# Kernel optimization log

Hardware: AMD Instinct MI355X
Metric: run time of the kernel (lower is better)

The kernel has to match this reference:

```python
import jax, jax.numpy as jnp
import numpy as np
import math

B, S, E, H, D = 2, 2048, 1024, 16, 64

def setup_inputs() -> dict:
    key = jax.random.key(0)
    ks = jax.random.split(key, 9)
    sc = 0.02
    return {
        "x": jax.random.normal(ks[0], (B, S, E), jnp.float32),
        "Wq": jax.random.normal(ks[1], (H, E, D), jnp.float32) * sc,
        "Wk": jax.random.normal(ks[2], (H, E, D), jnp.float32) * sc,
        "Wv": jax.random.normal(ks[3], (H, E, D), jnp.float32) * sc,
        "bq": jax.random.normal(ks[4], (H, D), jnp.float32) * sc,
        "bk": jax.random.normal(ks[5], (H, D), jnp.float32) * sc,
        "bv": jax.random.normal(ks[6], (H, D), jnp.float32) * sc,
        "Wo": jax.random.normal(ks[7], (H * D, E), jnp.float32) * sc,
        "bo": jax.random.normal(ks[8], (E,), jnp.float32) * sc,
    }

def reference(x, Wq, Wk, Wv, bq, bk, bv, Wo, bo):
    # per-head projections, batched over heads: [B,H,S,D]
    q = jnp.einsum('bse,hed->bhsd', x, Wq) + bq[None, :, None, :]
    k = jnp.einsum('bse,hed->bhsd', x, Wk) + bk[None, :, None, :]
    v = jnp.einsum('bse,hed->bhsd', x, Wv) + bv[None, :, None, :]
    # full score matrix [B,H,S,S], scaled by sqrt(head_size) as in original
    scores = jnp.einsum('bhqd,bhkd->bhqk', q, k) / math.sqrt(D)
    causal = jnp.tril(jnp.ones((S, S), bool))  # tril mask as in buffer
    scores = jnp.where(causal[None, None], scores, -jnp.inf)
    attn = jax.nn.softmax(scores, axis=-1)
    out = jnp.einsum('bhqk,bhkd->bhqd', attn, v)
    # concat heads in head order: [B,S,H*D]
    out = out.transpose(0, 2, 1, 3).reshape(B, S, H * D)
    # output projection (dropout is identity in eval / p=0)
    return out @ Wo + bo
```

## Files before the change

kernel.cpp:

```cpp
#include <hip/hip_runtime.h>

#define BB 2
#define SS 2048
#define EE 1024
#define HH 16
#define DD 64

typedef unsigned short u16;
typedef float f4 __attribute__((ext_vector_type(4)));
typedef __bf16 b8 __attribute__((ext_vector_type(8)));
typedef short s8i __attribute__((ext_vector_type(8)));
typedef u16 u16x4 __attribute__((ext_vector_type(4)));

__device__ inline u16 f2b(float f) {
  unsigned u = __builtin_bit_cast(unsigned, f);
  unsigned r = (u + 0x7fffu + ((u >> 16) & 1u)) >> 16;
  return (u16)r;
}

__global__ __launch_bounds__(256) void prep(const float* __restrict__ x,
                                            const float* __restrict__ Wq,
                                            const float* __restrict__ Wk,
                                            const float* __restrict__ Wv,
                                            const float* __restrict__ Wo,
                                            u16* __restrict__ xb,
                                            u16* __restrict__ Wt,
                                            u16* __restrict__ Wot) {
  int bid = blockIdx.x;
  int t = threadIdx.x;
  if (bid < 1024) {
    int i0 = bid * 256 + t;
    for (int j = 0; j < 4; ++j) {
      int i = i0 + j * 262144;
      f4 v = ((const f4*)x)[i];
      u16x4 o;
      for (int k2 = 0; k2 < 4; ++k2) o[k2] = f2b(v[k2]);
      ((u16x4*)xb)[i] = o;
    }
  } else if (bid < 1792) {
    __shared__ float tile[64][65];
    int z = bid - 1024;
    int y = z >> 4;
    int e0 = (z & 15) * 64;
    int qkv = y >> 4, h = y & 15;
    const float* W = (qkv == 0) ? Wq : (qkv == 1) ? Wk : Wv;
    for (int p = 0; p < 16; ++p) {
      int i = p * 4 + (t >> 6), d = t & 63;
      tile[i][d] = W[((size_t)h * EE + e0 + i) * DD + d];
    }
    __syncthreads();
    for (int p = 0; p < 16; ++p) {
      int d = p * 4 + (t >> 6), i = t & 63;
      Wt[((size_t)qkv * 1024 + h * 64 + d) * EE + e0 + i] = f2b(tile[i][d]);
    }
  } else {
    __shared__ float tile2[64][65];
    int z = bid - 1792;
    int e0 = (z & 15) * 64, c0 = (z >> 4) * 64;
    for (int p = 0; p < 16; ++p) {
      int i = p * 4 + (t >> 6), j = t & 63;
      tile2[i][j] = Wo[(size_t)(e0 + i) * (HH * DD) + c0 + j];
    }
    __syncthreads();
    for (int p = 0; p < 16; ++p) {
      int j = p * 4 + (t >> 6), i = t & 63;
      Wot[(size_t)(c0 + j) * EE + e0 + i] = f2b(tile2[i][j]);
    }
  }
}

__global__ __launch_bounds__(256) void gemmQKV(
    const u16* __restrict__ A, const u16* __restrict__ Bm,
    u16* __restrict__ Qo, u16* __restrict__ Ko, u16* __restrict__ Vo,
    const float* __restrict__ bq, const float* __restrict__ bk,
    const float* __restrict__ bv) {
  const int K = 1024;
  __shared__ u16 As[128 * 32];
  __shared__ u16 Bs[128 * 32];
  int t = threadIdx.x;
  int lane = t & 63, w = t >> 6;
  int wr = w >> 1, wc = w & 1;
  int lr = lane & 15, lg = lane >> 4;
  int m0 = blockIdx.y * 128, n0 = blockIdx.x * 128;

  f4 acc[4][4];
  const f4 z4 = {0.f, 0.f, 0.f, 0.f};
  for (int mi = 0; mi < 4; ++mi)
    for (int ni = 0; ni < 4; ++ni) acc[mi][ni] = z4;

  int r0 = t >> 2, s0 = t & 3;
  const u16* ga0 = A + (size_t)(m0 + r0) * K + s0 * 8;
  const u16* gb0 = Bm + (size_t)(n0 + r0) * K + s0 * 8;
  u16* la0 = As + w * 512;
  u16* la1 = As + 2048 + w * 512;
  u16* lb0 = Bs + w * 512;
  u16* lb1 = Bs + 2048 + w * 512;

  for (int ks = 0; ks < K / 32; ++ks) {
    int k0 = ks * 32;
    __builtin_amdgcn_global_load_lds(
        (const __attribute__((address_space(1))) void*)(ga0 + k0),
        (__attribute__((address_space(3))) void*)la0, 16, 0, 0);
    __builtin_amdgcn_global_load_lds(
        (const __attribute__((address_space(1))) void*)(ga0 + 64 * K + k0),
        (__attribute__((address_space(3))) void*)la1, 16, 0, 0);
    __builtin_amdgcn_global_load_lds(
        (const __attribute__((address_space(1))) void*)(gb0 + k0),
        (__attribute__((address_space(3))) void*)lb0, 16, 0, 0);
    __builtin_amdgcn_global_load_lds(
        (const __attribute__((address_space(1))) void*)(gb0 + 64 * K + k0),
        (__attribute__((address_space(3))) void*)lb1, 16, 0, 0);
    __syncthreads();
    b8 af[4], bf[4];
    for (int mi = 0; mi < 4; ++mi)
      af[mi] = *(const b8*)&As[(wr * 64 + mi * 16 + lr) * 32 + lg * 8];
    for (int ni = 0; ni < 4; ++ni)
      bf[ni] = *(const b8*)&Bs[(wc * 64 + ni * 16 + lr) * 32 + lg * 8];
    for (int mi = 0; mi < 4; ++mi)
      for (int ni = 0; ni < 4; ++ni)
        acc[mi][ni] = __builtin_amdgcn_mfma_f32_16x16x32_bf16(af[mi], bf[ni],
                                                              acc[mi][ni], 0, 0, 0);
    __syncthreads();
  }

  const float QSC = 0.18033688011112042f;
  for (int mi = 0; mi < 4; ++mi)
    for (int ni = 0; ni < 4; ++ni)
      for (int r = 0; r < 4; ++r) {
        int m_g = m0 + wr * 64 + mi * 16 + lg * 4 + r;
        int n_g = n0 + wc * 64 + ni * 16 + lr;
        float v = acc[mi][ni][r];
        int qkv = n_g >> 10, hd = n_g & 1023;
        const float* bias = (qkv == 0) ? bq : (qkv == 1) ? bk : bv;
        v += bias[hd];
        int b = m_g >> 11, s = m_g & 2047;
        int h = hd >> 6, d = hd & 63;
        if (qkv == 0) {
          Qo[(((size_t)b * HH + h) * SS + s) * DD + d] = f2b(v * QSC);
        } else if (qkv == 1) {
          Ko[(((size_t)b * HH + h) * SS + s) * DD + d] = f2b(v);
        } else {
          Vo[(((size_t)b * HH + h) * DD + d) * SS + s] = f2b(v);
        }
      }
}

__global__ __launch_bounds__(256) void gemmO(const u16* __restrict__ A,
                                             const u16* __restrict__ Bm,
                                             float* __restrict__ Co,
                                             const float* __restrict__ bo) {
  const int K = 1024;
  __shared__ u16 As[128 * 32];
  __shared__ u16 Bs[64 * 32];
  int t = threadIdx.x;
  int lane = t & 63, w = t >> 6;
  int lr = lane & 15, lg = lane >> 4;
  int m0 = blockIdx.y * 128, n0 = blockIdx.x * 64;

  f4 acc[2][4];
  const f4 z4 = {0.f, 0.f, 0.f, 0.f};
  for (int mi = 0; mi < 2; ++mi)
    for (int ni = 0; ni < 4; ++ni) acc[mi][ni] = z4;

  int r0 = t >> 2, s0 = t & 3;
  const u16* ga0 = A + (size_t)(m0 + r0) * K + s0 * 8;
  const u16* gb0 = Bm + (size_t)(n0 + r0) * K + s0 * 8;
  u16* la0 = As + w * 512;
  u16* la1 = As + 2048 + w * 512;
  u16* lb0 = Bs + w * 512;

  for (int ks = 0; ks < K / 32; ++ks) {
    int k0 = ks * 32;
    __builtin_amdgcn_global_load_lds(
        (const __attribute__((address_space(1))) void*)(ga0 + k0),
        (__attribute__((address_space(3))) void*)la0, 16, 0, 0);
    __builtin_amdgcn_global_load_lds(
        (const __attribute__((address_space(1))) void*)(ga0 + 64 * K + k0),
        (__attribute__((address_space(3))) void*)la1, 16, 0, 0);
    __builtin_amdgcn_global_load_lds(
        (const __attribute__((address_space(1))) void*)(gb0 + k0),
        (__attribute__((address_space(3))) void*)lb0, 16, 0, 0);
    __syncthreads();
    b8 af[2], bf[4];
    for (int mi = 0; mi < 2; ++mi)
      af[mi] = *(const b8*)&As[(w * 32 + mi * 16 + lr) * 32 + lg * 8];
    for (int ni = 0; ni < 4; ++ni)
      bf[ni] = *(const b8*)&Bs[(ni * 16 + lr) * 32 + lg * 8];
    for (int mi = 0; mi < 2; ++mi)
      for (int ni = 0; ni < 4; ++ni)
        acc[mi][ni] = __builtin_amdgcn_mfma_f32_16x16x32_bf16(af[mi], bf[ni],
                                                              acc[mi][ni], 0, 0, 0);
    __syncthreads();
  }

  for (int mi = 0; mi < 2; ++mi)
    for (int ni = 0; ni < 4; ++ni)
      for (int r = 0; r < 4; ++r) {
        int m_g = m0 + w * 32 + mi * 16 + lg * 4 + r;
        int n_g = n0 + ni * 16 + lr;
        Co[(size_t)m_g * 1024 + n_g] = acc[mi][ni][r] + bo[n_g];
      }
}

#define KST 72
#define PST 72
__global__ __launch_bounds__(256) void fattn(const u16* __restrict__ Qb,
                                             const u16* __restrict__ Kb,
                                             const u16* __restrict__ VTb,
                                             u16* __restrict__ AO) {
  __shared__ u16 Kl[2][64 * KST];
  __shared__ u16 Vl[2][64 * KST];
  __shared__ u16 Pl[4][16 * PST];

  int t = threadIdx.x, lane = t & 63, w = t >> 6;
  int lr = lane & 15, lg = lane >> 4;
  int bx = blockIdx.x, by = blockIdx.y;
  int qt = 31 - ((bx + by) & 31);
  int bh = by;
  int b = bh >> 4, h = bh & 15;
  size_t base = (size_t)bh * SS * DD;

  int r0 = t >> 2, s0 = t & 3;
  u16* kl0 = &Kl[0][r0 * KST + s0 * 8];
  u16* kl1 = &Kl[1][r0 * KST + s0 * 8];
  u16* vl0 = &Vl[0][r0 * KST + s0 * 8];
  u16* vl1 = &Vl[1][r0 * KST + s0 * 8];
  const u16* kg = Kb + base + (size_t)r0 * DD + s0 * 8;
  const u16* vg = VTb + base + (size_t)r0 * SS + s0 * 8;

  int qbase = qt * 64;
  int nt = qt + 1;

  const u16* qp = Qb + base + (size_t)(qbase + w * 16 + lr) * DD;
  b8 qf0 = *(const b8*)(qp + lg * 8);
  b8 qf1 = *(const b8*)(qp + 32 + lg * 8);

  const f4 z4 = {0.f, 0.f, 0.f, 0.f};
  f4 o[4];
  for (int i = 0; i < 4; ++i) o[i] = z4;
  float mrow[4], lsum[4];
  for (int r = 0; r < 4; ++r) { mrow[r] = -1e30f; lsum[r] = 0.f; }
  int qg = qbase + w * 16 + lg * 4;

  {
    *(s8i*)kl0 = *(const s8i*)(kg);
    *(s8i*)(kl0 + 32) = *(const s8i*)(kg + 32);
    *(s8i*)vl0 = *(const s8i*)(vg);
    *(s8i*)(vl0 + 32) = *(const s8i*)(vg + 32);
  }
  __syncthreads();

  for (int kt = 0; kt < nt; ++kt) {
    int cur = kt & 1;
    int kv0 = kt * 64;

    s8i nk0, nk1, nv0, nv1;
    bool more = (kt + 1 < nt);
    if (more) {
      const u16* kgn = kg + (size_t)(kv0 + 64) * DD;
      const u16* vgn = vg + kv0 + 64;
      nk0 = *(const s8i*)(kgn);
      nk1 = *(const s8i*)(kgn + 32);
      nv0 = *(const s8i*)(vgn);
      nv1 = *(const s8i*)(vgn + 32);
    }

    f4 sa[4];
    for (int n = 0; n < 4; ++n) sa[n] = z4;
    for (int n = 0; n < 4; ++n) {
      b8 kf0 = *(const b8*)&Kl[cur][(n * 16 + lr) * KST + lg * 8];
      b8 kf1 = *(const b8*)&Kl[cur][(n * 16 + lr) * KST + 32 + lg * 8];
      sa[n] = __builtin_amdgcn_mfma_f32_16x16x32_bf16(qf0, kf0, sa[n], 0, 0, 0);
      sa[n] = __builtin_amdgcn_mfma_f32_16x16x32_bf16(qf1, kf1, sa[n], 0, 0, 0);
    }

    if (kt == nt - 1) {
      for (int r = 0; r < 4; ++r) {
        int q = qg + r;
        if (kv0 + lr > q) sa[0][r] = -1e30f;
        if (kv0 + 16 + lr > q) sa[1][r] = -1e30f;
        if (kv0 + 32 + lr > q) sa[2][r] = -1e30f;
        if (kv0 + 48 + lr > q) sa[3][r] = -1e30f;
      }
    }

    float scl[4];
    for (int r = 0; r < 4; ++r) {
      float mx = fmaxf(fmaxf(sa[0][r], sa[1][r]), fmaxf(sa[2][r], sa[3][r]));
      mx = fmaxf(mx, __shfl_xor(mx, 1));
      mx = fmaxf(mx, __shfl_xor(mx, 2));
      mx = fmaxf(mx, __shfl_xor(mx, 4));
      mx = fmaxf(mx, __shfl_xor(mx, 8));
      float mn = fmaxf(mrow[r], mx);
      float sc = __builtin_amdgcn_exp2f(mrow[r] - mn);
      float p0 = __builtin_amdgcn_exp2f(sa[0][r] - mn);
      float p1 = __builtin_amdgcn_exp2f(sa[1][r] - mn);
      float p2 = __builtin_amdgcn_exp2f(sa[2][r] - mn);
      float p3 = __builtin_amdgcn_exp2f(sa[3][r] - mn);
      lsum[r] = lsum[r] * sc + ((p0 + p1) + (p2 + p3));
      mrow[r] = mn;
      scl[r] = sc;
      int prow = (lg * 4 + r) * PST;
      Pl[w][prow + lr] = f2b(p0);
      Pl[w][prow + 16 + lr] = f2b(p1);
      Pl[w][prow + 32 + lr] = f2b(p2);
      Pl[w][prow + 48 + lr] = f2b(p3);
    }
    for (int n = 0; n < 4; ++n) {
      f4 ov = o[n];
      for (int r = 0; r < 4; ++r) ov[r] *= scl[r];
      o[n] = ov;
    }

    b8 pf0 = *(const b8*)&Pl[w][lr * PST + lg * 8];
    b8 pf1 = *(const b8*)&Pl[w][lr * PST + 32 + lg * 8];
    for (int n = 0; n < 4; ++n) {
      b8 vf0 = *(const b8*)&Vl[cur][(n * 16 + lr) * KST + lg * 8];
      b8 vf1 = *(const b8*)&Vl[cur][(n * 16 + lr) * KST + 32 + lg * 8];
      o[n] = __builtin_amdgcn_mfma_f32_16x16x32_bf16(pf0, vf0, o[n], 0, 0, 0);
      o[n] = __builtin_amdgcn_mfma_f32_16x16x32_bf16(pf1, vf1, o[n], 0, 0, 0);
    }

    if (more) {
      u16* kln = cur ? kl0 : kl1;
      u16* vln = cur ? vl0 : vl1;
      *(s8i*)kln = nk0;
      *(s8i*)(kln + 32) = nk1;
      *(s8i*)vln = nv0;
      *(s8i*)(vln + 32) = nv1;
    }
    __syncthreads();
  }

  float rl[4];
  for (int r = 0; r < 4; ++r) {
    float s = lsum[r];
    s += __shfl_xor(s, 1);
    s += __shfl_xor(s, 2);
    s += __shfl_xor(s, 4);
    s += __shfl_xor(s, 8);
    rl[r] = 1.f / s;
  }
  for (int n = 0; n < 4; ++n)
    for (int r = 0; r < 4; ++r) {
      int qgr = qg + r;
      int d = n * 16 + lr;
      AO[((size_t)b * SS + qgr) * (HH * DD) + h * DD + d] = f2b(o[n][r] * rl[r]);
    }
}

extern "C" void kernel_launch(void* const* d_in, const int* in_sizes, int n_in,
                              void* d_out, int out_size, void* d_ws, size_t ws_size,
                              hipStream_t stream) {
  const float* x  = (const float*)d_in[0];
  const float* Wq = (const float*)d_in[1];
  const float* Wk = (const float*)d_in[2];
  const float* Wv = (const float*)d_in[3];
  const float* bq = (const float*)d_in[4];
  const float* bk = (const float*)d_in[5];
  const float* bv = (const float*)d_in[6];
  const float* Wo = (const float*)d_in[7];
  const float* bo = (const float*)d_in[8];

  char* ws = (char*)d_ws;
  u16* xb  = (u16*)(ws);
  u16* Wt  = (u16*)(ws + ((size_t)8 << 20));
  u16* Wot = (u16*)(ws + ((size_t)14 << 20));
  u16* Qw  = (u16*)(ws + ((size_t)16 << 20));
  u16* Kw  = (u16*)(ws + ((size_t)24 << 20));
  u16* VTw = (u16*)(ws + ((size_t)32 << 20));
  u16* AO  = xb;

  prep<<<2048, 256, 0, stream>>>(x, Wq, Wk, Wv, Wo, xb, Wt, Wot);
  gemmQKV<<<dim3(24, 32), 256, 0, stream>>>(xb, Wt, Qw, Kw, VTw, bq, bk, bv);
  fattn<<<dim3(32, 32), 256, 0, stream>>>(Qw, Kw, VTw, AO);
  gemmO<<<dim3(16, 32), 256, 0, stream>>>(AO, Wot, (float*)d_out, bo);
}
```

Measured before the change: 238.5 us.

## Compute V projection transposed and pair causal query tiles per attention block

The QKV GEMM now computes the V part as Wv^T times x^T, so the transposed V output is written with contiguous stores along the sequence dimension instead of strided scatter. The attention kernel launches half as many blocks, and each block processes query tile 31-x followed by tile x, which evens out the causal workload per block. This halves the number of attention blocks, which may reduce overlap between blocks. The V path also reads different bias indices and tile mapping, and correctness depends on that mapping being right.

New measurement: 423.7 us. 77.7% more time.

```diff
diff --git a/kernel.cpp b/kernel.cpp
--- a/kernel.cpp
+++ b/kernel.cpp
@@ -70,7 +70,7 @@
 }
 
 __global__ __launch_bounds__(256) void gemmQKV(
-    const u16* __restrict__ A, const u16* __restrict__ Bm,
+    const u16* __restrict__ xb, const u16* __restrict__ Wt,
     u16* __restrict__ Qo, u16* __restrict__ Ko, u16* __restrict__ Vo,
     const float* __restrict__ bq, const float* __restrict__ bk,
     const float* __restrict__ bv) {
@@ -81,7 +81,23 @@
   int lane = t & 63, w = t >> 6;
   int wr = w >> 1, wc = w & 1;
   int lr = lane & 15, lg = lane >> 4;
-  int m0 = blockIdx.y * 128, n0 = blockIdx.x * 128;
+
+  int bid = blockIdx.x;
+  bool isV = bid >= 512;
+  int m0, n0;
+  const u16 *Ap, *Bp;
+  if (!isV) {
+    m0 = (bid >> 4) * 128;
+    n0 = (bid & 15) * 128;
+    Ap = xb;
+    Bp = Wt;
+  } else {
+    int z = bid - 512;
+    m0 = (z >> 5) * 128;
+    n0 = (z & 31) * 128;
+    Ap = Wt + (size_t)2048 * 1024;
+    Bp = xb;
+  }
 
   f4 acc[4][4];
   const f4 z4 = {0.f, 0.f, 0.f, 0.f};
@@ -89,8 +105,8 @@
     for (int ni = 0; ni < 4; ++ni) acc[mi][ni] = z4;
 
   int r0 = t >> 2, s0 = t & 3;
-  const u16* ga0 = A + (size_t)(m0 + r0) * K + s0 * 8;
-  const u16* gb0 = Bm + (size_t)(n0 + r0) * K + s0 * 8;
+  const u16* ga0 = Ap + (size_t)(m0 + r0) * K + s0 * 8;
+  const u16* gb0 = Bp + (size_t)(n0 + r0) * K + s0 * 8;
   u16* la0 = As + w * 512;
   u16* la1 = As + 2048 + w * 512;
   u16* lb0 = Bs + w * 512;
@@ -130,17 +146,20 @@
         int m_g = m0 + wr * 64 + mi * 16 + lg * 4 + r;
         int n_g = n0 + wc * 64 + ni * 16 + lr;
         float v = acc[mi][ni][r];
-        int qkv = n_g >> 10, hd = n_g & 1023;
-        const float* bias = (qkv == 0) ? bq : (qkv == 1) ? bk : bv;
-        v += bias[hd];
-        int b = m_g >> 11, s = m_g & 2047;
-        int h = hd >> 6, d = hd & 63;
-        if (qkv == 0) {
-          Qo[(((size_t)b * HH + h) * SS + s) * DD + d] = f2b(v * QSC);
-        } else if (qkv == 1) {
-          Ko[(((size_t)b * HH + h) * SS + s) * DD + d] = f2b(v);
+        if (!isV) {
+          int qkv = n_g >> 10, hd = n_g & 1023;
+          v += (qkv == 0) ? bq[hd] : bk[hd];
+          int b = m_g >> 11, s = m_g & 2047;
+          int h = hd >> 6, d = hd & 63;
+          if (qkv == 0) {
+            Qo[(((size_t)b * HH + h) * SS + s) * DD + d] = f2b(v * QSC);
+          } else {
+            Ko[(((size_t)b * HH + h) * SS + s) * DD + d] = f2b(v);
+          }
         } else {
-          Vo[(((size_t)b * HH + h) * DD + d) * SS + s] = f2b(v);
+          v += bv[m_g];
+          int b = n_g >> 11, s = n_g & 2047;
+          Vo[(((size_t)b * HH + (m_g >> 6)) * DD + (m_g & 63)) * SS + s] = f2b(v);
         }
       }
 }
@@ -214,9 +233,7 @@
 
   int t = threadIdx.x, lane = t & 63, w = t >> 6;
   int lr = lane & 15, lg = lane >> 4;
-  int bx = blockIdx.x, by = blockIdx.y;
-  int qt = 31 - ((bx + by) & 31);
-  int bh = by;
+  int bh = blockIdx.y;
   int b = bh >> 4, h = bh & 15;
   size_t base = (size_t)bh * SS * DD;
 
@@ -228,125 +245,129 @@
   const u16* kg = Kb + base + (size_t)r0 * DD + s0 * 8;
   const u16* vg = VTb + base + (size_t)r0 * SS + s0 * 8;
 
-  int qbase = qt * 64;
-  int nt = qt + 1;
-
-  const u16* qp = Qb + base + (size_t)(qbase + w * 16 + lr) * DD;
-  b8 qf0 = *(const b8*)(qp + lg * 8);
-  b8 qf1 = *(const b8*)(qp + 32 + lg * 8);
-
-  const f4 z4 = {0.f, 0.f, 0.f, 0.f};
-  f4 o[4];
-  for (int i = 0; i < 4; ++i) o[i] = z4;
-  float mrow[4], lsum[4];
-  for (int r = 0; r < 4; ++r) { mrow[r] = -1e30f; lsum[r] = 0.f; }
-  int qg = qbase + w * 16 + lg * 4;
-
-  {
-    *(s8i*)kl0 = *(const s8i*)(kg);
-    *(s8i*)(kl0 + 32) = *(const s8i*)(kg + 32);
-    *(s8i*)vl0 = *(const s8i*)(vg);
-    *(s8i*)(vl0 + 32) = *(const s8i*)(vg + 32);
-  }
-  __syncthreads();
-
-  for (int kt = 0; kt < nt; ++kt) {
-    int cur = kt & 1;
-    int kv0 = kt * 64;
-
-    s8i nk0, nk1, nv0, nv1;
-    bool more = (kt + 1 < nt);
-    if (more) {
-      const u16* kgn = kg + (size_t)(kv0 + 64) * DD;
-      const u16* vgn = vg + kv0 + 64;
-      nk0 = *(const s8i*)(kgn);
-      nk1 = *(const s8i*)(kgn + 32);
-      nv0 = *(const s8i*)(vgn);
-      nv1 = *(const s8i*)(vgn + 32);
-    }
-
-    f4 sa[4];
-    for (int n = 0; n < 4; ++n) sa[n] = z4;
-    for (int n = 0; n < 4; ++n) {
-      b8 kf0 = *(const b8*)&Kl[cur][(n * 16 + lr) * KST + lg * 8];
-      b8 kf1 = *(const b8*)&Kl[cur][(n * 16 + lr) * KST + 32 + lg * 8];
-      sa[n] = __builtin_amdgcn_mfma_f32_16x16x32_bf16(qf0, kf0, sa[n], 0, 0, 0);
-      sa[n] = __builtin_amdgcn_mfma_f32_16x16x32_bf16(qf1, kf1, sa[n], 0, 0, 0);
-    }
-
-    if (kt == nt - 1) {
+  for (int half = 0; half < 2; ++half) {
+    int qt = half ? blockIdx.x : 31 - blockIdx.x;
+    int qbase = qt * 64;
+    int nt = qt + 1;
+
+    const u16* qp = Qb + base + (size_t)(qbase + w * 16 + lr) * DD;
+    b8 qf0 = *(const b8*)(qp + lg * 8);
+    b8 qf1 = *(const b8*)(qp + 32 + lg * 8);
+
+    const f4 z4 = {0.f, 0.f, 0.f, 0.f};
+    f4 o[4];
+    for (int i = 0; i < 4; ++i) o[i] = z4;
+    float mrow[4], lsum[4];
+    for (int r = 0; r < 4; ++r) { mrow[r] = -1e30f; lsum[r] = 0.f; }
+    int qg = qbase + w * 16 + lg * 4;
+
+    {
+      *(s8i*)kl0 = *(const s8i*)(kg);
+      *(s8i*)(kl0 + 32) = *(const s8i*)(kg + 32);
+      *(s8i*)vl0 = *(const s8i*)(vg);
+      *(s8i*)(vl0 + 32) = *(const s8i*)(vg + 32);
+    }
+    __syncthreads();
+
+    for (int kt = 0; kt < nt; ++kt) {
+      int cur = kt & 1;
+      int kv0 = kt * 64;
+
+      s8i nk0, nk1, nv0, nv1;
+      bool more = (kt + 1 < nt);
+      if (more) {
+        const u16* kgn = kg + (size_t)(kv0 + 64) * DD;
+        const u16* vgn = vg + kv0 + 64;
+        nk0 = *(const s8i*)(kgn);
+        nk1 = *(const s8i*)(kgn + 32);
+        nv0 = *(const s8i*)(vgn);
+        nv1 = *(const s8i*)(vgn + 32);
+      }
+
+      f4 sa[4];
+      for (int n = 0; n < 4; ++n) sa[n] = z4;
+      for (int n = 0; n < 4; ++n) {
+        b8 kf0 = *(const b8*)&Kl[cur][(n * 16 + lr) * KST + lg * 8];
+        b8 kf1 = *(const b8*)&Kl[cur][(n * 16 + lr) * KST + 32 + lg * 8];
+        sa[n] = __builtin_amdgcn_mfma_f32_16x16x32_bf16(qf0, kf0, sa[n], 0, 0, 0);
+        sa[n] = __builtin_amdgcn_mfma_f32_16x16x32_bf16(qf1, kf1, sa[n], 0, 0, 0);
+      }
+
+      if (kt == nt - 1) {
+        for (int r = 0; r < 4; ++r) {
+          int q = qg + r;
+          if (kv0 + lr > q) sa[0][r] = -1e30f;
+          if (kv0 + 16 + lr > q) sa[1][r] = -1e30f;
+          if (kv0 + 32 + lr > q) sa[2][r] = -1e30f;
+          if (kv0 + 48 + lr > q) sa[3][r] = -1e30f;
+        }
+      }
+
+      float scl[4];
       for (int r = 0; r < 4; ++r) {
-        int q = qg + r;
-        if (kv0 + lr > q) sa[0][r] = -1e30f;
-        if (kv0 + 16 + lr > q) sa[1][r] = -1e30f;
-        if (kv0 + 32 + lr > q) sa[2][r] = -1e30f;
-        if (kv0 + 48 + lr > q) sa[3][r] = -1e30f;
-      }
-    }
-
-    float scl[4];
+        float mx = fmaxf(fmaxf(sa[0][r], sa[1][r]), fmaxf(sa[2][r], sa[3][r]));
+        mx = fmaxf(mx, __shfl_xor(mx, 1));
+        mx = fmaxf(mx, __shfl_xor(mx, 2));
+        mx = fmaxf(mx, __shfl_xor(mx, 4));
+        mx = fmaxf(mx, __shfl_xor(mx, 8));
+        float mn = fmaxf(mrow[r], mx);
+        float sc = __builtin_amdgcn_exp2f(mrow[r] - mn);
+        float p0 = __builtin_amdgcn_exp2f(sa[0][r] - mn);
+        float p1 = __builtin_amdgcn_exp2f(sa[1][r] - mn);
+        float p2 = __builtin_amdgcn_exp2f(sa[2][r] - mn);
+        float p3 = __builtin_amdgcn_exp2f(sa[3][r] - mn);
+        lsum[r] = lsum[r] * sc + ((p0 + p1) + (p2 + p3));
+        mrow[r] = mn;
+        scl[r] = sc;
+        int prow = (lg * 4 + r) * PST;
+        Pl[w][prow + lr] = f2b(p0);
+        Pl[w][prow + 16 + lr] = f2b(p1);
+        Pl[w][prow + 32 + lr] = f2b(p2);
+        Pl[w][prow + 48 + lr] = f2b(p3);
+      }
+      for (int n = 0; n < 4; ++n) {
+        f4 ov = o[n];
+        for (int r = 0; r < 4; ++r) ov[r] *= scl[r];
+        o[n] = ov;
+      }
+
+      b8 pf0 = *(const b8*)&Pl[w][lr * PST + lg * 8];
+      b8 pf1 = *(const b8*)&Pl[w][lr * PST + 32 + lg * 8];
+      for (int n = 0; n < 4; ++n) {
+        b8 vf0 = *(const b8*)&Vl[cur][(n * 16 + lr) * KST + lg * 8];
+        b8 vf1 = *(const b8*)&Vl[cur][(n * 16 + lr) * KST + 32 + lg * 8];
+        o[n] = __builtin_amdgcn_mfma_f32_16x16x32_bf16(pf0, vf0, o[n], 0, 0, 0);
+        o[n] = __builtin_amdgcn_mfma_f32_16x16x32_bf16(pf1, vf1, o[n], 0, 0, 0);
+      }
+
+      if (more) {
+        u16* kln = cur ? kl0 : kl1;
+        u16* vln = cur ? vl0 : vl1;
+        *(s8i*)kln = nk0;
+        *(s8i*)(kln + 32) = nk1;
+        *(s8i*)vln = nv0;
+        *(s8i*)(vln + 32) = nv1;
+      }
+      __syncthreads();
+    }
+
+    float rl[4];
     for (int r = 0; r < 4; ++r) {
-      float mx = fmaxf(fmaxf(sa[0][r], sa[1][r]), fmaxf(sa[2][r], sa[3][r]));
-      mx = fmaxf(mx, __shfl_xor(mx, 1));
-      mx = fmaxf(mx, __shfl_xor(mx, 2));
-      mx = fmaxf(mx, __shfl_xor(mx, 4));
-      mx = fmaxf(mx, __shfl_xor(mx, 8));
-      float mn = fmaxf(mrow[r], mx);
-      float sc = __builtin_amdgcn_exp2f(mrow[r] - mn);
-      float p0 = __builtin_amdgcn_exp2f(sa[0][r] - mn);
-      float p1 = __builtin_amdgcn_exp2f(sa[1][r] - mn);
-      float p2 = __builtin_amdgcn_exp2f(sa[2][r] - mn);
-      float p3 = __builtin_amdgcn_exp2f(sa[3][r] - mn);
-      lsum[r] = lsum[r] * sc + ((p0 + p1) + (p2 + p3));
-      mrow[r] = mn;
-      scl[r] = sc;
-      int prow = (lg * 4 + r) * PST;
-      Pl[w][prow + lr] = f2b(p0);
-      Pl[w][prow + 16 + lr] = f2b(p1);
-      Pl[w][prow + 32 + lr] = f2b(p2);
-      Pl[w][prow + 48 + lr] = f2b(p3);
-    }
-    for (int n = 0; n < 4; ++n) {
-      f4 ov = o[n];
-      for (int r = 0; r < 4; ++r) ov[r] *= scl[r];
-      o[n] = ov;
-    }
-
-    b8 pf0 = *(const b8*)&Pl[w][lr * PST + lg * 8];
-    b8 pf1 = *(const b8*)&Pl[w][lr * PST + 32 + lg * 8];
-    for (int n = 0; n < 4; ++n) {
-      b8 vf0 = *(const b8*)&Vl[cur][(n * 16 + lr) * KST + lg * 8];
-      b8 vf1 = *(const b8*)&Vl[cur][(n * 16 + lr) * KST + 32 + lg * 8];
-      o[n] = __builtin_amdgcn_mfma_f32_16x16x32_bf16(pf0, vf0, o[n], 0, 0, 0);
-      o[n] = __builtin_amdgcn_mfma_f32_16x16x32_bf16(pf1, vf1, o[n], 0, 0, 0);
-    }
-
-    if (more) {
-      u16* kln = cur ? kl0 : kl1;
-      u16* vln = cur ? vl0 : vl1;
-      *(s8i*)kln = nk0;
-      *(s8i*)(kln + 32) = nk1;
-      *(s8i*)vln = nv0;
-      *(s8i*)(vln + 32) = nv1;
-    }
-    __syncthreads();
-  }
-
-  float rl[4];
-  for (int r = 0; r < 4; ++r) {
-    float s = lsum[r];
-    s += __shfl_xor(s, 1);
-    s += __shfl_xor(s, 2);
-    s += __shfl_xor(s, 4);
-    s += __shfl_xor(s, 8);
-    rl[r] = 1.f / s;
-  }
-  for (int n = 0; n < 4; ++n)
-    for (int r = 0; r < 4; ++r) {
-      int qgr = qg + r;
-      int d = n * 16 + lr;
-      AO[((size_t)b * SS + qgr) * (HH * DD) + h * DD + d] = f2b(o[n][r] * rl[r]);
-    }
+      float s = lsum[r];
+      s += __shfl_xor(s, 1);
+      s += __shfl_xor(s, 2);
+      s += __shfl_xor(s, 4);
+      s += __shfl_xor(s, 8);
+      rl[r] = 1.f / s;
+    }
+    for (int n = 0; n < 4; ++n)
+      for (int r = 0; r < 4; ++r) {
+        int qgr = qg + r;
+        int d = n * 16 + lr;
+        AO[((size_t)b * SS + qgr) * (HH * DD) + h * DD + d] = f2b(o[n][r] * rl[r]);
+      }
+    __syncthreads();
+  }
 }
 
 extern "C" void kernel_launch(void* const* d_in, const int* in_sizes, int n_in,
@@ -372,7 +393,7 @@
   u16* AO  = xb;
 
   prep<<<2048, 256, 0, stream>>>(x, Wq, Wk, Wv, Wo, xb, Wt, Wot);
-  gemmQKV<<<dim3(24, 32), 256, 0, stream>>>(xb, Wt, Qw, Kw, VTw, bq, bk, bv);
-  fattn<<<dim3(32, 32), 256, 0, stream>>>(Qw, Kw, VTw, AO);
+  gemmQKV<<<768, 256, 0, stream>>>(xb, Wt, Qw, Kw, VTw, bq, bk, bv);
+  fattn<<<dim3(16, 32), 256, 0, stream>>>(Qw, Kw, VTw, AO);
   gemmO<<<dim3(16, 32), 256, 0, stream>>>(AO, Wot, (float*)d_out, bo);
 }
```
